# Kernel tuning notes

Hardware: AMD Instinct MI355X
Metric: run time of the kernel (lower is better)

The kernel has to match this reference:

```python
import jax, jax.numpy as jnp
import numpy as np

B, C, H, W = 4, 64, 64, 64
CQK = C // 8


def setup_inputs() -> dict:
    key = jax.random.key(0)
    k0, k1, k2, k3, k4 = jax.random.split(key, 5)
    x = jax.random.normal(k0, (B, C, H, W), dtype=jnp.float32)
    # Conv1d kernel_size=1, bias=False -> plain [out, in] matmul weights
    Wq = jax.random.normal(k1, (CQK, C), dtype=jnp.float32) * 0.05
    Wk = jax.random.normal(k2, (CQK, C), dtype=jnp.float32) * 0.05
    Wv = jax.random.normal(k3, (C, C), dtype=jnp.float32) * 0.05
    # torch init is 0; use a nonzero scalar so the attention path is exercised
    gamma = jax.random.uniform(k4, (1,), dtype=jnp.float32)
    return {"x": x, "Wq": Wq, "Wk": Wk, "Wv": Wv, "gamma": gamma}


def reference(x, Wq, Wk, Wv, gamma):
    shape = x.shape                      # [B, C, H, W]
    xf = x.reshape(shape[0], shape[1], -1)  # [B, C, N]
    q = jnp.einsum('oc,bcn->bon', Wq, xf)   # [B, C/8, N]
    k = jnp.einsum('oc,bcn->bon', Wk, xf)   # [B, C/8, N]
    v = jnp.einsum('oc,bcn->bon', Wv, xf)   # [B, C, N]
    # score[b, n, m] = sum_c q[b, c, n] * k[b, c, m]  (no 1/sqrt(d) scale)
    score = jnp.einsum('bcn,bcm->bnm', q, k)  # [B, N, N]
    # unconventional softmax over dim=1 (rows/first N axis, i.e. per-column)
    score = jax.nn.softmax(score, axis=1)
    out = jnp.einsum('bcn,bnm->bcm', v, score)  # [B, C, N]
    attention = gamma * out + xf
    return attention.reshape(shape)
```

## Files before the change

### kernel.cpp

```cpp
#include <hip/hip_runtime.h>

#define BB 4
#define NN 4096

typedef __attribute__((ext_vector_type(8))) short short8v;
typedef __attribute__((ext_vector_type(4))) short short4v;
typedef __attribute__((ext_vector_type(4))) float float4v;

__device__ __forceinline__ unsigned short f2bf_rn(float f) {
    unsigned u = __float_as_uint(f);
    u += 0x7FFFu + ((u >> 16) & 1u);
    return (unsigned short)(u >> 16);
}

__device__ __forceinline__ unsigned pack2_rte(float fa, float fb) {
    unsigned a = __float_as_uint(fa), b = __float_as_uint(fb);
    a = a + 0x7FFFu + ((a >> 16) & 1u);
    b = b + 0x7FFFu + ((b >> 16) & 1u);
    return __builtin_amdgcn_perm(b, a, 0x07060302u);
}

__global__ __launch_bounds__(256) void qkv_kernel(
    const float* __restrict__ x,
    const float* __restrict__ Wq, const float* __restrict__ Wk,
    const float* __restrict__ Wv,
    unsigned short* __restrict__ Qt, unsigned short* __restrict__ Kt,
    unsigned short* __restrict__ Vsw)
{
    __shared__ float xs[64][36];
    __shared__ float wl[64][81];
    __shared__ unsigned short Ot[80][40];

    const int t  = threadIdx.x;
    const int b  = blockIdx.y;
    const int nb = blockIdx.x;
    const int n0 = nb * 32;

    #pragma unroll
    for (int i = 0; i < 20; ++i) {
        int idx = t + 256 * i;
        int r = idx >> 6, c = idx & 63;
        float w;
        if (r < 8)       w = Wq[r * 64 + c];
        else if (r < 16) w = Wk[(r - 8) * 64 + c];
        else             w = Wv[(r - 16) * 64 + c];
        wl[c][r] = w;
    }
    #pragma unroll
    for (int i = 0; i < 2; ++i) {
        int idx = t + 256 * i;
        int c = idx >> 3, n4 = (idx & 7) * 4;
        *(float4*)&xs[c][n4] = *(const float4*)&x[(size_t)(b * 64 + c) * NN + n0 + n4];
    }
    __syncthreads();

    const int n2 = (t & 15) * 2;
    const int og = t >> 4;

    float acc[5][2];
    #pragma unroll
    for (int k = 0; k < 5; ++k) { acc[k][0] = 0.f; acc[k][1] = 0.f; }

    for (int c = 0; c < 64; ++c) {
        float2 xv = *(const float2*)&xs[c][n2];
        #pragma unroll
        for (int k = 0; k < 5; ++k) {
            float wv = wl[c][og * 5 + k];
            acc[k][0] += wv * xv.x;
            acc[k][1] += wv * xv.y;
        }
    }

    #pragma unroll
    for (int k = 0; k < 5; ++k) {
        Ot[og * 5 + k][n2]     = f2bf_rn(acc[k][0]);
        Ot[og * 5 + k][n2 + 1] = f2bf_rn(acc[k][1]);
    }
    __syncthreads();

    if (t < 64) {
        int n = t & 31;
        int rbase = (t < 32) ? 0 : 8;
        short8v p;
        #pragma unroll
        for (int j = 0; j < 8; ++j) p[j] = (short)Ot[rbase + j][n];
        unsigned short* dst = ((t < 32) ? Qt : Kt) + ((size_t)b * NN + n0 + n) * 8;
        *(short8v*)dst = p;
    }

    {
        int ct = t >> 6, l = t & 63;
        unsigned short* cb = Vsw + ((size_t)(b * 4 + ct) * 128 + nb) * 512;
        short8v d = *(short8v*)&Ot[16 + ct * 16 + (l & 15)][(l >> 4) * 8];
        *(short8v*)(cb + l * 8) = d;
    }
}

union AttnSmem {
    unsigned short Pb[4][2][16][40];
    float Ored[4][64][17];
};

__global__ __launch_bounds__(256, 4) void attn_kernel(
    const unsigned short* __restrict__ Qt,
    const unsigned short* __restrict__ Kt,
    const unsigned short* __restrict__ Vsw,
    const float* __restrict__ x, const float* __restrict__ gamma,
    float* __restrict__ out)
{
    __shared__ __align__(16) AttnSmem sm;
    __shared__ float Lred[4][16];
    __shared__ float Lf[16];

    const int t    = threadIdx.x;
    const int w    = t >> 6;
    const int lane = t & 63;
    const int quad = lane >> 4;
    const int l15  = lane & 15;
    const int b    = blockIdx.y;
    const int m0   = blockIdx.x * 16;

    const short8v zfrag = {0, 0, 0, 0, 0, 0, 0, 0};
    const float4v zacc  = {0.f, 0.f, 0.f, 0.f};

    short8v bk = zfrag;
    if (quad == 0)
        bk = *(const short8v*)(Kt + (size_t)(b * NN + m0 + l15) * 8);

    float4v acc[4];
    #pragma unroll
    for (int ct = 0; ct < 4; ++ct) acc[ct] = zacc;
    float Lacc = 0.f;

    const unsigned short* qrow = Qt + (size_t)(b * NN + w * 1024 + l15) * 8;
    const unsigned short* vptr = Vsw + ((size_t)b * 4 * 128 + w * 32) * 512 + lane * 8;

    short8v av0 = *(const short8v*)(vptr);
    short8v av1 = *(const short8v*)(vptr + 1 * 128 * 512);
    short8v av2 = *(const short8v*)(vptr + 2 * 128 * 512);
    short8v av3 = *(const short8v*)(vptr + 3 * 128 * 512);
    {
        short8v aq0 = zfrag, aq1 = zfrag;
        if (quad == 0) {
            aq0 = *(const short8v*)(qrow);
            aq1 = *(const short8v*)(qrow + 16 * 8);
        }
        float4v s0 = __builtin_amdgcn_mfma_f32_16x16x32_bf16(aq0, bk, zacc, 0, 0, 0);
        float4v s1 = __builtin_amdgcn_mfma_f32_16x16x32_bf16(aq1, bk, zacc, 0, 0, 0);
        float p[8];
        #pragma unroll
        for (int j = 0; j < 4; ++j) { p[j] = __expf(s0[j]); p[4 + j] = __expf(s1[j]); }
        #pragma unroll
        for (int j = 0; j < 8; ++j) Lacc += p[j];
        unsigned pk0 = pack2_rte(p[0], p[1]), pk1 = pack2_rte(p[2], p[3]);
        unsigned pk2 = pack2_rte(p[4], p[5]), pk3 = pack2_rte(p[6], p[7]);
        *(uint2*)&sm.Pb[w][0][l15][quad * 4]      = make_uint2(pk0, pk1);
        *(uint2*)&sm.Pb[w][0][l15][16 + quad * 4] = make_uint2(pk2, pk3);
    }
    short8v avn0 = *(const short8v*)(vptr + 512);
    short8v avn1 = *(const short8v*)(vptr + 1 * 128 * 512 + 512);
    short8v avn2 = *(const short8v*)(vptr + 2 * 128 * 512 + 512);
    short8v avn3 = *(const short8v*)(vptr + 3 * 128 * 512 + 512);
    short8v aqn0 = zfrag, aqn1 = zfrag;
    if (quad == 0) {
        aqn0 = *(const short8v*)(qrow + 32 * 8);
        aqn1 = *(const short8v*)(qrow + 48 * 8);
    }

    for (int it = 0; it < 31; ++it) {
        const int itn = it + 1;
        const int i2  = (it + 2) & 31;

        short8v bp = *(const short8v*)&sm.Pb[w][it & 1][l15][quad * 8];

        float4v s0 = __builtin_amdgcn_mfma_f32_16x16x32_bf16(aqn0, bk, zacc, 0, 0, 0);
        float4v s1 = __builtin_amdgcn_mfma_f32_16x16x32_bf16(aqn1, bk, zacc, 0, 0, 0);

        short8v a2q0 = zfrag, a2q1 = zfrag;
        if (quad == 0) {
            a2q0 = *(const short8v*)(qrow + (size_t)(i2 * 32) * 8);
            a2q1 = *(const short8v*)(qrow + (size_t)(i2 * 32 + 16) * 8);
        }
        short8v a2v0 = *(const short8v*)(vptr + i2 * 512);
        short8v a2v1 = *(const short8v*)(vptr + 1 * 128 * 512 + i2 * 512);
        short8v a2v2 = *(const short8v*)(vptr + 2 * 128 * 512 + i2 * 512);
        short8v a2v3 = *(const short8v*)(vptr + 3 * 128 * 512 + i2 * 512);

        float p[8];
        #pragma unroll
        for (int j = 0; j < 4; ++j) { p[j] = __expf(s0[j]); p[4 + j] = __expf(s1[j]); }
        #pragma unroll
        for (int j = 0; j < 8; ++j) Lacc += p[j];
        unsigned pk0 = pack2_rte(p[0], p[1]), pk1 = pack2_rte(p[2], p[3]);
        unsigned pk2 = pack2_rte(p[4], p[5]), pk3 = pack2_rte(p[6], p[7]);
        *(uint2*)&sm.Pb[w][itn & 1][l15][quad * 4]      = make_uint2(pk0, pk1);
        *(uint2*)&sm.Pb[w][itn & 1][l15][16 + quad * 4] = make_uint2(pk2, pk3);

        acc[0] = __builtin_amdgcn_mfma_f32_16x16x32_bf16(av0, bp, acc[0], 0, 0, 0);
        acc[1] = __builtin_amdgcn_mfma_f32_16x16x32_bf16(av1, bp, acc[1], 0, 0, 0);
        acc[2] = __builtin_amdgcn_mfma_f32_16x16x32_bf16(av2, bp, acc[2], 0, 0, 0);
        acc[3] = __builtin_amdgcn_mfma_f32_16x16x32_bf16(av3, bp, acc[3], 0, 0, 0);

        av0 = avn0; av1 = avn1; av2 = avn2; av3 = avn3;
        avn0 = a2v0; avn1 = a2v1; avn2 = a2v2; avn3 = a2v3;
        aqn0 = a2q0; aqn1 = a2q1;
    }

    {
        short8v bp = *(const short8v*)&sm.Pb[w][1][l15][quad * 8];
        acc[0] = __builtin_amdgcn_mfma_f32_16x16x32_bf16(av0, bp, acc[0], 0, 0, 0);
        acc[1] = __builtin_amdgcn_mfma_f32_16x16x32_bf16(av1, bp, acc[1], 0, 0, 0);
        acc[2] = __builtin_amdgcn_mfma_f32_16x16x32_bf16(av2, bp, acc[2], 0, 0, 0);
        acc[3] = __builtin_amdgcn_mfma_f32_16x16x32_bf16(av3, bp, acc[3], 0, 0, 0);
    }

    Lacc += __shfl_xor(Lacc, 16, 64);
    Lacc += __shfl_xor(Lacc, 32, 64);
    if (lane < 16) Lred[w][lane] = Lacc;

    __syncthreads();

    #pragma unroll
    for (int ct = 0; ct < 4; ++ct)
        #pragma unroll
        for (int r = 0; r < 4; ++r)
            sm.Ored[w][ct * 16 + quad * 4 + r][l15] = acc[ct][r];
    if (t < 16)
        Lf[t] = 1.f / (Lred[0][t] + Lred[1][t] + Lred[2][t] + Lred[3][t]);
    __syncthreads();

    {
        const float gv = gamma[0];
        int c = t >> 2, m4 = (t & 3) * 4;
        float4 o;
        #pragma unroll
        for (int i = 0; i < 4; ++i) {
            float s = sm.Ored[0][c][m4 + i] + sm.Ored[1][c][m4 + i]
                    + sm.Ored[2][c][m4 + i] + sm.Ored[3][c][m4 + i];
            ((float*)&o)[i] = s * Lf[m4 + i];
        }
        size_t gbase = (size_t)(b * 64 + c) * NN + m0 + m4;
        float4 xv = *(const float4*)&x[gbase];
        float4 r;
        r.x = gv * o.x + xv.x; r.y = gv * o.y + xv.y;
        r.z = gv * o.z + xv.z; r.w = gv * o.w + xv.w;
        *(float4*)&out[gbase] = r;
    }
}

extern "C" void kernel_launch(void* const* d_in, const int* in_sizes, int n_in,
                              void* d_out, int out_size, void* d_ws, size_t ws_size,
                              hipStream_t stream) {
    const float* x     = (const float*)d_in[0];
    const float* Wq    = (const float*)d_in[1];
    const float* Wk    = (const float*)d_in[2];
    const float* Wv    = (const float*)d_in[3];
    const float* gamma = (const float*)d_in[4];
    float* out = (float*)d_out;

    unsigned short* ws = (unsigned short*)d_ws;
    unsigned short* Qt  = ws;
    unsigned short* Kt  = Qt + (size_t)BB * NN * 8;
    unsigned short* Vsw = Kt + (size_t)BB * NN * 8;

    qkv_kernel<<<dim3(NN / 32, BB), 256, 0, stream>>>(x, Wq, Wk, Wv, Qt, Kt, Vsw);
    attn_kernel<<<dim3(NN / 16, BB), 256, 0, stream>>>(Qt, Kt, Vsw, x, gamma, out);
}
```

Measured before the change: 97.76 us.

## Split attention key dimension four ways with partial outputs and reduce kernel

The attention kernel now splits the 4096-long reduction over source positions into 4 chunks. Each block handles 8 chunks per wave instead of 32 and writes unnormalized partial outputs and partial softmax denominators to workspace. A new reduce kernel sums the partials, applies the normalization, gamma and the residual, and writes the output. This gives four times as many blocks with shorter loops, in exchange for an extra launch, pipeline prologue overhead repeated per block, and about 16 MB of partial-output traffic written and read back.

```diff
diff --git a/kernel.cpp b/kernel.cpp
--- a/kernel.cpp
+++ b/kernel.cpp
@@ -2,6 +2,7 @@
 
 #define BB 4
 #define NN 4096
+#define NCH 8
 
 typedef __attribute__((ext_vector_type(8))) short short8v;
 typedef __attribute__((ext_vector_type(4))) short short4v;
@@ -105,20 +106,20 @@
     const unsigned short* __restrict__ Qt,
     const unsigned short* __restrict__ Kt,
     const unsigned short* __restrict__ Vsw,
-    const float* __restrict__ x, const float* __restrict__ gamma,
-    float* __restrict__ out)
+    float* __restrict__ Opart, float* __restrict__ Lpart)
 {
     __shared__ __align__(16) AttnSmem sm;
     __shared__ float Lred[4][16];
-    __shared__ float Lf[16];
 
     const int t    = threadIdx.x;
     const int w    = t >> 6;
     const int lane = t & 63;
     const int quad = lane >> 4;
     const int l15  = lane & 15;
-    const int b    = blockIdx.y;
-    const int m0   = blockIdx.x * 16;
+    const int mt   = blockIdx.x;
+    const int s    = blockIdx.y;
+    const int b    = blockIdx.z;
+    const int m0   = mt * 16;
 
     const short8v zfrag = {0, 0, 0, 0, 0, 0, 0, 0};
     const float4v zacc  = {0.f, 0.f, 0.f, 0.f};
@@ -132,8 +133,9 @@
     for (int ct = 0; ct < 4; ++ct) acc[ct] = zacc;
     float Lacc = 0.f;
 
-    const unsigned short* qrow = Qt + (size_t)(b * NN + w * 1024 + l15) * 8;
-    const unsigned short* vptr = Vsw + ((size_t)b * 4 * 128 + w * 32) * 512 + lane * 8;
+    const int cbase = (s * 4 + w) * NCH;
+    const unsigned short* qrow = Qt + ((size_t)b * NN + cbase * 32 + l15) * 8;
+    const unsigned short* vptr = Vsw + ((size_t)b * 4 * 128 + cbase) * 512 + lane * 8;
 
     short8v av0 = *(const short8v*)(vptr);
     short8v av1 = *(const short8v*)(vptr + 1 * 128 * 512);
@@ -167,9 +169,9 @@
         aqn1 = *(const short8v*)(qrow + 48 * 8);
     }
 
-    for (int it = 0; it < 31; ++it) {
+    for (int it = 0; it < NCH - 1; ++it) {
         const int itn = it + 1;
-        const int i2  = (it + 2) & 31;
+        const int i2  = (it + 2) & (NCH - 1);
 
         short8v bp = *(const short8v*)&sm.Pb[w][it & 1][l15][quad * 8];
 
@@ -225,27 +227,59 @@
         #pragma unroll
         for (int r = 0; r < 4; ++r)
             sm.Ored[w][ct * 16 + quad * 4 + r][l15] = acc[ct][r];
-    if (t < 16)
-        Lf[t] = 1.f / (Lred[0][t] + Lred[1][t] + Lred[2][t] + Lred[3][t]);
-    __syncthreads();
-
+    __syncthreads();
+
+    const size_t blk = ((size_t)(b * 4 + s) * 256 + mt);
     {
-        const float gv = gamma[0];
         int c = t >> 2, m4 = (t & 3) * 4;
         float4 o;
         #pragma unroll
         for (int i = 0; i < 4; ++i) {
-            float s = sm.Ored[0][c][m4 + i] + sm.Ored[1][c][m4 + i]
-                    + sm.Ored[2][c][m4 + i] + sm.Ored[3][c][m4 + i];
-            ((float*)&o)[i] = s * Lf[m4 + i];
+            ((float*)&o)[i] = sm.Ored[0][c][m4 + i] + sm.Ored[1][c][m4 + i]
+                            + sm.Ored[2][c][m4 + i] + sm.Ored[3][c][m4 + i];
         }
-        size_t gbase = (size_t)(b * 64 + c) * NN + m0 + m4;
-        float4 xv = *(const float4*)&x[gbase];
-        float4 r;
-        r.x = gv * o.x + xv.x; r.y = gv * o.y + xv.y;
-        r.z = gv * o.z + xv.z; r.w = gv * o.w + xv.w;
-        *(float4*)&out[gbase] = r;
-    }
+        *(float4*)&Opart[blk * 1024 + c * 16 + m4] = o;
+    }
+    if (t < 16)
+        Lpart[blk * 16 + t] = Lred[0][t] + Lred[1][t] + Lred[2][t] + Lred[3][t];
+}
+
+__global__ __launch_bounds__(256) void reduce_kernel(
+    const float* __restrict__ Opart, const float* __restrict__ Lpart,
+    const float* __restrict__ x, const float* __restrict__ gamma,
+    float* __restrict__ out)
+{
+    __shared__ float Lf[16];
+    const int t  = threadIdx.x;
+    const int mt = blockIdx.x;
+    const int b  = blockIdx.y;
+    const int m0 = mt * 16;
+
+    if (t < 16) {
+        float l = 0.f;
+        #pragma unroll
+        for (int s = 0; s < 4; ++s)
+            l += Lpart[((size_t)(b * 4 + s) * 256 + mt) * 16 + t];
+        Lf[t] = 1.f / l;
+    }
+    __syncthreads();
+
+    const float gv = gamma[0];
+    const int c = t >> 2, m4 = (t & 3) * 4;
+    float4 o = {0.f, 0.f, 0.f, 0.f};
+    #pragma unroll
+    for (int s = 0; s < 4; ++s) {
+        float4 p = *(const float4*)&Opart[((size_t)(b * 4 + s) * 256 + mt) * 1024 + c * 16 + m4];
+        o.x += p.x; o.y += p.y; o.z += p.z; o.w += p.w;
+    }
+    size_t gbase = (size_t)(b * 64 + c) * NN + m0 + m4;
+    float4 xv = *(const float4*)&x[gbase];
+    float4 r;
+    r.x = gv * o.x * Lf[m4 + 0] + xv.x;
+    r.y = gv * o.y * Lf[m4 + 1] + xv.y;
+    r.z = gv * o.z * Lf[m4 + 2] + xv.z;
+    r.w = gv * o.w * Lf[m4 + 3] + xv.w;
+    *(float4*)&out[gbase] = r;
 }
 
 extern "C" void kernel_launch(void* const* d_in, const int* in_sizes, int n_in,
@@ -262,7 +296,10 @@
     unsigned short* Qt  = ws;
     unsigned short* Kt  = Qt + (size_t)BB * NN * 8;
     unsigned short* Vsw = Kt + (size_t)BB * NN * 8;
+    float* Opart = (float*)(Vsw + (size_t)BB * 4 * 128 * 512);
+    float* Lpart = Opart + (size_t)4096 * 1024;
 
     qkv_kernel<<<dim3(NN / 32, BB), 256, 0, stream>>>(x, Wq, Wk, Wv, Qt, Kt, Vsw);
-    attn_kernel<<<dim3(NN / 16, BB), 256, 0, stream>>>(Qt, Kt, Vsw, x, gamma, out);
-}
+    attn_kernel<<<dim3(NN / 16, 4, BB), 256, 0, stream>>>(Qt, Kt, Vsw, Opart, Lpart);
+    reduce_kernel<<<dim3(NN / 16, BB), 256, 0, stream>>>(Opart, Lpart, x, gamma, out);
+}
```

Measured after the change: 112.2 us. 1.15x slower.
